# Kernel optimization log

Hardware: AMD Instinct MI355X
Metric: run time of the kernel (lower is better)

Reference implementation:

```python
import jax, jax.numpy as jnp
import numpy as np

F = 20            # number of fields
V_FIELD = 5000    # vocab per field
TOTAL = F * V_FIELD
D = 64            # embedding dim (emd)
B = 8192          # batch
OFFSETS = jnp.arange(F, dtype=jnp.int32) * V_FIELD  # field offsets into shared table
_iu, _ju = np.triu_indices(F, k=1)                  # P = F*(F-1)/2 = 190 pairs
I_IDX = jnp.asarray(_iu, dtype=jnp.int32)
J_IDX = jnp.asarray(_ju, dtype=jnp.int32)


def setup_inputs() -> dict:
    key = jax.random.key(0)
    k1, k2, k3 = jax.random.split(key, 3)
    x = jax.random.randint(k1, (B, F), 0, V_FIELD, dtype=jnp.int32)
    # F field-aware embedding tables, each over the full offset vocab
    W = jax.random.normal(k2, (F, TOTAL, D), dtype=jnp.float32) * 0.01
    # linear term table (emd=1)
    Wl = jax.random.normal(k3, (TOTAL, 1), dtype=jnp.float32) * 0.01
    bias = jnp.zeros((1,), dtype=jnp.float32)
    return {"x": x, "W": W, "Wl": Wl, "bias": bias}


def reference(x, W, Wl, bias):
    idx = x + OFFSETS[None, :]                      # [B, F] global ids
    # embedding[:, j*F+i] == table j looked up at field-i's id
    a = W[J_IDX[None, :], idx[:, I_IDX]]            # [B, P, D] = V_j[x_i]
    b = W[I_IDX[None, :], idx[:, J_IDX]]            # [B, P, D] = V_i[x_j]
    interaction = jnp.sum(a * b, axis=(1, 2))[:, None]  # [B, 1]
    lin = Wl[idx].sum(axis=1)                       # [B, 1]
    return jax.nn.sigmoid(lin + bias + interaction)
```

## Files before the change

kernel.cpp:

```cpp
#include <hip/hip_runtime.h>
#include <math.h>


#define FF 20
#define V_FIELD 5000
#define TOT (FF * V_FIELD)
#define DD 64
#define NB 8192
#define NP 190
#define GPG 4
#define NG 48
#define SCH 256
#define NCH (NB / SCH)
#define NWORK (NG * NCH)
#define GRID 512

__global__ __launch_bounds__(256) void ffm_pairs(
    const int* __restrict__ x,
    const float* __restrict__ W,
    float* __restrict__ acc)
{
    __shared__ short pi[GPG * NG], pj[GPG * NG];
    __shared__ int gidx[SCH * FF];

    const int t = threadIdx.x;

    if (t < GPG * NG) {
        int pp = (t >= NP) ? 0 : t;
        int i = 0;
        while (pp >= FF - 1 - i) { pp -= FF - 1 - i; ++i; }
        pi[t] = (short)i;
        pj[t] = (short)(i + 1 + pp);
    }

    const int wv   = t >> 6;
    const int ln   = t & 63;
    const int grp  = ln >> 4;
    const int sub  = ln & 15;
    const char* Wb = (const char*)W;

    for (int w = blockIdx.x; w < NWORK; w += GRID) {
        const int g_id  = w / NCH;
        const int chunk = w % NCH;

        __syncthreads();
        for (int k = t; k < SCH * FF; k += 256) {
            const int f = k % FF;
            gidx[k] = x[chunk * (SCH * FF) + k] + f * V_FIELD;
        }
        __syncthreads();

#pragma unroll 2
        for (int q = 0; q < 16; ++q) {
            const int sl = wv * 64 + q * 4 + grp;
            float4 a4 = make_float4(0.f, 0.f, 0.f, 0.f);
#pragma unroll
            for (int k = 0; k < GPG; ++k) {
                const int p = g_id * GPG + k;
                if (p < NP) {
                    const int i = pi[p], j = pj[p];
                    const unsigned ga = (unsigned)gidx[sl * FF + i];
                    const unsigned gb = (unsigned)gidx[sl * FF + j];
                    const float4 va = *(const float4*)
                        (Wb + (((unsigned)(j * TOT) + ga) << 8) + sub * 16);
                    const float4 vb = *(const float4*)
                        (Wb + (((unsigned)(i * TOT) + gb) << 8) + sub * 16);
                    a4.x = fmaf(va.x, vb.x, a4.x);
                    a4.y = fmaf(va.y, vb.y, a4.y);
                    a4.z = fmaf(va.z, vb.z, a4.z);
                    a4.w = fmaf(va.w, vb.w, a4.w);
                }
            }
            float s = (a4.x + a4.y) + (a4.z + a4.w);
            s += __shfl_xor(s, 1, 64);
            s += __shfl_xor(s, 2, 64);
            s += __shfl_xor(s, 4, 64);
            s += __shfl_xor(s, 8, 64);
            if (sub == 0)
                atomicAdd(&acc[chunk * SCH + sl], s);
        }
    }
}

__global__ __launch_bounds__(256) void ffm_finish(
    const int* __restrict__ x,
    const float* __restrict__ Wl,
    const float* __restrict__ bias,
    const float* __restrict__ acc,
    float* __restrict__ out)
{
    const int b = blockIdx.x * 256 + threadIdx.x;
    float s = acc[b];
    const int* xr = x + b * FF;
#pragma unroll
    for (int f = 0; f < FF; ++f)
        s += Wl[xr[f] + f * V_FIELD];
    out[b] = 1.f / (1.f + expf(-(s + bias[0])));
}

extern "C" void kernel_launch(void* const* d_in, const int* in_sizes, int n_in,
                              void* d_out, int out_size, void* d_ws, size_t ws_size,
                              hipStream_t stream) {
    const int*   x    = (const int*)d_in[0];
    const float* W    = (const float*)d_in[1];
    const float* Wl   = (const float*)d_in[2];
    const float* bias = (const float*)d_in[3];
    float* out = (float*)d_out;
    float* acc = (float*)d_ws;

    hipMemsetAsync(acc, 0, NB * sizeof(float), stream);
    hipLaunchKernelGGL(ffm_pairs, dim3(GRID), dim3(256), 0, stream, x, W, acc);
    hipLaunchKernelGGL(ffm_finish, dim3(NB / 256), dim3(256), 0, stream,
                       x, Wl, bias, acc, out);
}
```

Measured before the change: 691.3 us.

## Remap FFM pair kernel to one-shot blocks with register-accumulated pair groups

Replaces the grid-stride loop over (pair-group, 256-sample chunk) work items with a fixed grid of 128 sample chunks times 16 pair-group sets. Each block loads 64 samples' indices once and loops over 3 pair groups, keeping four float4 accumulators in registers. Reductions and atomics then run once per sample per block instead of once per pair group, which cuts atomic traffic and repeated index staging. The trade-offs are a larger grid of 2048 blocks, a launch-bounds occupancy hint, and more gather loads issued per thread before any reduction.

```diff
diff --git a/kernel.cpp b/kernel.cpp
--- a/kernel.cpp
+++ b/kernel.cpp
@@ -5,23 +5,23 @@
 #define FF 20
 #define V_FIELD 5000
 #define TOT (FF * V_FIELD)
-#define DD 64
 #define NB 8192
 #define NP 190
 #define GPG 4
 #define NG 48
-#define SCH 256
-#define NCH (NB / SCH)
-#define NWORK (NG * NCH)
-#define GRID 512
+#define SPB 64
+#define NCH (NB / SPB)
+#define NSET 16
+#define NITEM (NG / NSET)
+#define GRID (NCH * NSET)
 
-__global__ __launch_bounds__(256) void ffm_pairs(
+__global__ __launch_bounds__(256, 4) void ffm_pairs(
     const int* __restrict__ x,
     const float* __restrict__ W,
     float* __restrict__ acc)
 {
     __shared__ short pi[GPG * NG], pj[GPG * NG];
-    __shared__ int gidx[SCH * FF];
+    __shared__ int gidx[SPB * FF];
 
     const int t = threadIdx.x;
 
@@ -33,30 +33,33 @@
         pj[t] = (short)(i + 1 + pp);
     }
 
-    const int wv   = t >> 6;
-    const int ln   = t & 63;
-    const int grp  = ln >> 4;
-    const int sub  = ln & 15;
+    const int set = blockIdx.x >> 7;
+    const int c   = blockIdx.x & (NCH - 1);
+
+    for (int k = t; k < SPB * FF; k += 256) {
+        const int f = k % FF;
+        gidx[k] = x[c * (SPB * FF) + k] + f * V_FIELD;
+    }
+    __syncthreads();
+
+    const int wv  = t >> 6;
+    const int ln  = t & 63;
+    const int grp = ln >> 4;
+    const int sub = ln & 15;
     const char* Wb = (const char*)W;
 
-    for (int w = blockIdx.x; w < NWORK; w += GRID) {
-        const int g_id  = w / NCH;
-        const int chunk = w % NCH;
+    float4 a4[4];
+#pragma unroll
+    for (int q = 0; q < 4; ++q) a4[q] = make_float4(0.f, 0.f, 0.f, 0.f);
 
-        __syncthreads();
-        for (int k = t; k < SCH * FF; k += 256) {
-            const int f = k % FF;
-            gidx[k] = x[chunk * (SCH * FF) + k] + f * V_FIELD;
-        }
-        __syncthreads();
-
-#pragma unroll 2
-        for (int q = 0; q < 16; ++q) {
-            const int sl = wv * 64 + q * 4 + grp;
-            float4 a4 = make_float4(0.f, 0.f, 0.f, 0.f);
+    for (int item = 0; item < NITEM; ++item) {
+        const int g = set + item * NSET;
+#pragma unroll
+        for (int q = 0; q < 4; ++q) {
+            const int sl = wv * 16 + q * 4 + grp;
 #pragma unroll
             for (int k = 0; k < GPG; ++k) {
-                const int p = g_id * GPG + k;
+                const int p = g * GPG + k;
                 if (p < NP) {
                     const int i = pi[p], j = pj[p];
                     const unsigned ga = (unsigned)gidx[sl * FF + i];
@@ -65,20 +68,24 @@
                         (Wb + (((unsigned)(j * TOT) + ga) << 8) + sub * 16);
                     const float4 vb = *(const float4*)
                         (Wb + (((unsigned)(i * TOT) + gb) << 8) + sub * 16);
-                    a4.x = fmaf(va.x, vb.x, a4.x);
-                    a4.y = fmaf(va.y, vb.y, a4.y);
-                    a4.z = fmaf(va.z, vb.z, a4.z);
-                    a4.w = fmaf(va.w, vb.w, a4.w);
+                    a4[q].x = fmaf(va.x, vb.x, a4[q].x);
+                    a4[q].y = fmaf(va.y, vb.y, a4[q].y);
+                    a4[q].z = fmaf(va.z, vb.z, a4[q].z);
+                    a4[q].w = fmaf(va.w, vb.w, a4[q].w);
                 }
             }
-            float s = (a4.x + a4.y) + (a4.z + a4.w);
-            s += __shfl_xor(s, 1, 64);
-            s += __shfl_xor(s, 2, 64);
-            s += __shfl_xor(s, 4, 64);
-            s += __shfl_xor(s, 8, 64);
-            if (sub == 0)
-                atomicAdd(&acc[chunk * SCH + sl], s);
         }
+    }
+
+#pragma unroll
+    for (int q = 0; q < 4; ++q) {
+        float s = (a4[q].x + a4[q].y) + (a4[q].z + a4[q].w);
+        s += __shfl_xor(s, 1, 64);
+        s += __shfl_xor(s, 2, 64);
+        s += __shfl_xor(s, 4, 64);
+        s += __shfl_xor(s, 8, 64);
+        if (sub == 0)
+            atomicAdd(&acc[c * SPB + wv * 16 + q * 4 + grp], s);
     }
 }
 
```

Result: faster. 663.4 us (-4.0%).
